# Optimization experiments

Measured on AMD Instinct MI355X. Metric: run time of the kernel, lower is better.

Reference implementation:

```python
import jax, jax.numpy as jnp
import numpy as np

D_MODEL = 2048
N_HEADS = 16
Q_LORA = 1536
KV_LORA = 512
NOPE = 128
ROPE = 64
D_QK = NOPE + ROPE  # 192
D_V = 128
D_FF = 8192
BATCH = 2
SEQ = 2048
THETA = 10000.0
EPS = 1e-5


def rms_norm(x, w=None, eps=EPS):
    y = x * jax.lax.rsqrt(jnp.mean(x * x, axis=-1, keepdims=True) + eps)
    return y * w if w is not None else y


def apply_rope(x, cos, sin):
    # x: [B,S,H,D] with D even; pairs are consecutive (view_as_complex semantics)
    xr, xi = x[..., 0::2], x[..., 1::2]            # [B,S,H,D/2]
    c = cos[None, :, None, :]
    s = sin[None, :, None, :]
    yr = xr * c - xi * s
    yi = xr * s + xi * c
    return jnp.stack([yr, yi], axis=-1).reshape(x.shape)


def setup_inputs() -> dict:
    key = jax.random.key(0)
    ks = jax.random.split(key, 12)
    sd = 0.02
    inv_freq = 1.0 / (THETA ** (np.arange(0, ROPE, 2, dtype=np.float32) / ROPE))
    freqs = np.outer(np.arange(SEQ, dtype=np.float32), inv_freq)  # [S, ROPE/2]
    return {
        "hidden_states": jax.random.normal(ks[0], (BATCH, SEQ, D_MODEL), jnp.float32),
        "sequence_mask": jnp.ones((BATCH, SEQ), jnp.int32),
        "freqs_cos": jnp.asarray(np.cos(freqs)),
        "freqs_sin": jnp.asarray(np.sin(freqs)),
        "ln1_w": jnp.ones((D_MODEL,), jnp.float32),
        "ln2_w": jnp.ones((D_MODEL,), jnp.float32),
        "Wq_down": jax.random.normal(ks[1], (D_MODEL, Q_LORA), jnp.float32) * sd,
        "Wq_up": jax.random.normal(ks[2], (Q_LORA, N_HEADS * D_QK), jnp.float32) * sd,
        "Wkv_down": jax.random.normal(ks[3], (D_MODEL, KV_LORA + ROPE), jnp.float32) * sd,
        "Wkv_up": jax.random.normal(ks[4], (KV_LORA, N_HEADS * (NOPE + D_V)), jnp.float32) * sd,
        "Wo": jax.random.normal(ks[5], (N_HEADS * D_V, D_MODEL), jnp.float32) * sd,
        "Wgate": jax.random.normal(ks[6], (D_MODEL, D_FF), jnp.float32) * sd,
        "Wup": jax.random.normal(ks[7], (D_MODEL, D_FF), jnp.float32) * sd,
        "Wdown": jax.random.normal(ks[8], (D_FF, D_MODEL), jnp.float32) * sd,
    }


def reference(hidden_states, sequence_mask, freqs_cos, freqs_sin, ln1_w, ln2_w,
              Wq_down, Wq_up, Wkv_down, Wkv_up, Wo, Wgate, Wup, Wdown):
    B, S, _ = hidden_states.shape
    residual = hidden_states
    h = rms_norm(hidden_states, ln1_w)

    # --- MLA attention ---
    q_latent = rms_norm(h @ Wq_down)                       # [B,S,q_lora]
    q = (q_latent @ Wq_up).reshape(B, S, N_HEADS, D_QK)
    q_nope, q_rope = q[..., :NOPE], q[..., NOPE:]
    q_rope = apply_rope(q_rope, freqs_cos, freqs_sin)
    q = jnp.concatenate([q_rope, q_nope], axis=-1)         # [B,S,H,192]

    kv_lr = h @ Wkv_down                                   # [B,S,kv_lora+rope]
    kv_latent, k_rope = kv_lr[..., :KV_LORA], kv_lr[..., KV_LORA:]
    k_rope = apply_rope(k_rope[:, :, None, :], freqs_cos, freqs_sin)  # [B,S,1,64]
    k_rope = jnp.broadcast_to(k_rope, (B, S, N_HEADS, ROPE))
    kv = (rms_norm(kv_latent) @ Wkv_up)                    # [B,S,H*(nope+v)]
    k_nope = kv[..., :N_HEADS * NOPE].reshape(B, S, N_HEADS, NOPE)
    v = kv[..., N_HEADS * NOPE:].reshape(B, S, N_HEADS, D_V)
    k = jnp.concatenate([k_rope, k_nope], axis=-1)         # [B,S,H,192]

    scale = 1.0 / jnp.sqrt(jnp.float32(D_QK))
    scores = jnp.einsum('bqhd,bkhd->bhqk', q, k) * scale   # [B,H,S,S]
    seq_ok = (sequence_mask > 0)
    causal = jnp.tril(jnp.ones((S, S), bool))
    mask = causal[None, None] & seq_ok[:, None, None, :]
    scores = jnp.where(mask, scores, jnp.float32(-1e30))
    probs = jax.nn.softmax(scores, axis=-1)
    attn = jnp.einsum('bhqk,bkhd->bqhd', probs, v)         # [B,S,H,128]
    attn_out = attn.reshape(B, S, N_HEADS * D_V) @ Wo

    x = residual + attn_out

    # --- dense GLU MLP ---
    h2 = rms_norm(x, ln2_w)
    mlp_out = (jax.nn.silu(h2 @ Wgate) * (h2 @ Wup)) @ Wdown
    return x + mlp_out
```

## Files before the change

### kernel.cpp

```cpp
#include <hip/hip_runtime.h>
#include <hip/hip_bf16.h>
#include <stdint.h>

#define B_    2
#define S_    2048
#define H_    16
#define DM    2048
#define QL    1536
#define KVL   512
#define NOPE_ 128
#define ROPE_ 64
#define DQK   192
#define DV    128
#define DFF   8192
#define NT    (B_ * S_)
#define EPS_  1e-5f

typedef __bf16 bf16x8 __attribute__((ext_vector_type(8)));
typedef float  f32x4  __attribute__((ext_vector_type(4)));

__device__ __forceinline__ unsigned short f2bf(float f) {
  union { float f; uint32_t u; } v; v.f = f;
  uint32_t r = v.u + 0x7fffu + ((v.u >> 16) & 1u);
  return (unsigned short)(r >> 16);
}
__device__ __forceinline__ float bf2f(unsigned short h) {
  union { uint32_t u; float f; } v; v.u = ((uint32_t)h) << 16;
  return v.f;
}
__device__ __forceinline__ float ldv(float x) { return x; }
__device__ __forceinline__ float ldv(unsigned short x) { return bf2f(x); }

__device__ __forceinline__ void g2l16(const unsigned short* g, unsigned short* l) {
  __builtin_amdgcn_global_load_lds((const __attribute__((address_space(1))) unsigned int*)g,
                                   (__attribute__((address_space(3))) unsigned int*)l,
                                   16, 0, 0);
}

__global__ __launch_bounds__(256) void wt_kernel(const float* __restrict__ W,
                                                 unsigned short* __restrict__ Wt,
                                                 int K, int N) {
  __shared__ unsigned short tile[32][33];
  int kt = blockIdx.y * 32, nt = blockIdx.x * 32;
  int tx = threadIdx.x & 31, ty = threadIdx.x >> 5;
#pragma unroll
  for (int kk = 0; kk < 32; kk += 8)
    tile[kk + ty][tx] = f2bf(W[(size_t)(kt + kk + ty) * N + nt + tx]);
  __syncthreads();
#pragma unroll
  for (int nn = 0; nn < 32; nn += 8)
    Wt[(size_t)(nt + nn + ty) * K + kt + tx] = tile[tx][nn + ty];
}

template <typename TIN>
__global__ __launch_bounds__(256) void rms_kernel(const TIN* __restrict__ in,
                                                  unsigned short* __restrict__ out,
                                                  const float* __restrict__ w,
                                                  int D, int ldin) {
  int row = blockIdx.x, tid = threadIdx.x;
  const TIN* rp = in + (size_t)row * ldin;
  float ss = 0.f;
  for (int i = tid; i < D; i += 256) { float v = ldv(rp[i]); ss += v * v; }
#pragma unroll
  for (int off = 32; off >= 1; off >>= 1) ss += __shfl_xor(ss, off);
  __shared__ float red[4];
  if ((tid & 63) == 0) red[tid >> 6] = ss;
  __syncthreads();
  ss = red[0] + red[1] + red[2] + red[3];
  float rs = rsqrtf(ss / (float)D + EPS_);
  unsigned short* op = out + (size_t)row * D;
  for (int i = tid; i < D; i += 256) {
    float v = ldv(rp[i]) * rs;
    if (w) v *= w[i];
    op[i] = f2bf(v);
  }
}

template <int MODE>
__global__ __launch_bounds__(256) void gemm128(const unsigned short* __restrict__ A,
                                               const unsigned short* __restrict__ Bt,
                                               void* C, const float* __restrict__ addsrc,
                                               int M, int N, int K) {
  __shared__ unsigned short As[128 * 32];
  __shared__ unsigned short Bs[128 * 32];
  int tid = threadIdx.x, lane = tid & 63, wave = tid >> 6;
  int quad = lane >> 4, l16 = lane & 15;
  int wm = wave >> 1, wn = wave & 1;
  int m0 = blockIdx.y * 128, n0 = blockIdx.x * 128;

  int f0 = tid * 8;
  int rs0 = f0 >> 5, cs0 = f0 & 31;
  const unsigned short* Ag0 = A + (size_t)(m0 + rs0) * K + cs0;
  const unsigned short* Ag1 = A + (size_t)(m0 + 64 + rs0) * K + cs0;
  const unsigned short* Bg0 = Bt + (size_t)(n0 + rs0) * K + cs0;
  const unsigned short* Bg1 = Bt + (size_t)(n0 + 64 + rs0) * K + cs0;

  const unsigned short* ArdBase = As + quad * 8 + (wm * 64 + l16) * 32;
  const unsigned short* BrdBase = Bs + quad * 8 + (wn * 64 + l16) * 32;

  f32x4 ac[4][4] = {};
  for (int k = 0; k < K; k += 32) {
    __syncthreads();
    g2l16(Ag0 + k, (unsigned short*)As + f0);
    g2l16(Ag1 + k, (unsigned short*)As + 2048 + f0);
    g2l16(Bg0 + k, (unsigned short*)Bs + f0);
    g2l16(Bg1 + k, (unsigned short*)Bs + 2048 + f0);
    __syncthreads();
    bf16x8 af[4], bfr[4];
#pragma unroll
    for (int mt = 0; mt < 4; ++mt) af[mt]  = *(const bf16x8*)(ArdBase + mt * 16 * 32);
#pragma unroll
    for (int nt = 0; nt < 4; ++nt) bfr[nt] = *(const bf16x8*)(BrdBase + nt * 16 * 32);
#pragma unroll
    for (int mt = 0; mt < 4; ++mt)
#pragma unroll
      for (int nt = 0; nt < 4; ++nt)
        ac[mt][nt] = __builtin_amdgcn_mfma_f32_16x16x32_bf16(af[mt], bfr[nt], ac[mt][nt], 0, 0, 0);
  }

#pragma unroll
  for (int mt = 0; mt < 4; ++mt)
#pragma unroll
    for (int nt = 0; nt < 4; ++nt)
#pragma unroll
      for (int r = 0; r < 4; ++r) {
        int row = m0 + wm * 64 + mt * 16 + quad * 4 + r;
        int col = n0 + wn * 64 + nt * 16 + l16;
        size_t idx = (size_t)row * N + col;
        float v = ac[mt][nt][r];
        if (MODE == 0)      ((unsigned short*)C)[idx] = f2bf(v);
        else if (MODE == 1) ((float*)C)[idx] = v;
        else                ((float*)C)[idx] = addsrc[idx] + v;
      }
}

template <int MODE>
__global__ __launch_bounds__(256) void gemm_kernel(const unsigned short* __restrict__ A,
                                                   const unsigned short* __restrict__ Bt,
                                                   void* C, const float* addsrc,
                                                   int M, int N, int K) {
  int lane = threadIdx.x & 63, wave = threadIdx.x >> 6;
  int quad = lane >> 4, l16 = lane & 15;
  int row0 = blockIdx.y * 64 + wave * 16;
  int col0 = blockIdx.x * 64;
  const unsigned short* Ap = A + (size_t)(row0 + l16) * K + quad * 8;
  const unsigned short* Bp = Bt + (size_t)(col0 + l16) * K + quad * 8;
  size_t bs16 = (size_t)16 * K;
  f32x4 ac[4] = {};
  for (int k = 0; k < K; k += 32) {
    bf16x8 a = *(const bf16x8*)(Ap + k);
#pragma unroll
    for (int t = 0; t < 4; ++t) {
      bf16x8 b = *(const bf16x8*)(Bp + bs16 * t + k);
      ac[t] = __builtin_amdgcn_mfma_f32_16x16x32_bf16(a, b, ac[t], 0, 0, 0);
    }
  }
#pragma unroll
  for (int t = 0; t < 4; ++t)
#pragma unroll
    for (int r = 0; r < 4; ++r) {
      int row = row0 + quad * 4 + r, col = col0 + t * 16 + l16;
      size_t idx = (size_t)row * N + col;
      float v = ac[t][r];
      if (MODE == 0)      ((unsigned short*)C)[idx] = f2bf(v);
      else if (MODE == 1) ((float*)C)[idx] = v;
      else                ((float*)C)[idx] = addsrc[idx] + v;
    }
}

__global__ __launch_bounds__(256) void silumul_kernel(const unsigned short* __restrict__ g,
                                                      const unsigned short* __restrict__ u,
                                                      unsigned short* __restrict__ o, int n8) {
  int i = blockIdx.x * 256 + threadIdx.x;
  if (i >= n8) return;
  uint4 gv = ((const uint4*)g)[i];
  uint4 uv = ((const uint4*)u)[i];
  const unsigned short* gp = (const unsigned short*)&gv;
  const unsigned short* up = (const unsigned short*)&uv;
  uint4 ov;
  unsigned short* op = (unsigned short*)&ov;
#pragma unroll
  for (int j = 0; j < 8; ++j) {
    float gf = bf2f(gp[j]), uf = bf2f(up[j]);
    float s = gf / (1.f + __expf(-gf));
    op[j] = f2bf(s * uf);
  }
  ((uint4*)o)[i] = ov;
}

__global__ __launch_bounds__(256) void build_q_kernel(const unsigned short* __restrict__ qg,
                                                      const float* __restrict__ fcos,
                                                      const float* __restrict__ fsin,
                                                      unsigned short* __restrict__ qo) {
  const float SCALE = 0.07216878364870323f;
  int idx = blockIdx.x * 256 + threadIdx.x;
  if (idx >= NT * H_ * 96) return;
  int i = idx % 96, t = idx / 96;
  int h = t % H_, bs = t / H_, s = bs % S_;
  const unsigned short* src = qg + (size_t)bs * (H_ * DQK) + h * DQK;
  unsigned short* dst = qo + ((size_t)bs * H_ + h) * DQK;
  if (i < 32) {
    float xr = bf2f(src[NOPE_ + 2 * i]), xi = bf2f(src[NOPE_ + 2 * i + 1]);
    float c = fcos[s * 32 + i], sn = fsin[s * 32 + i];
    dst[2 * i]     = f2bf((xr * c - xi * sn) * SCALE);
    dst[2 * i + 1] = f2bf((xr * sn + xi * c) * SCALE);
  } else {
    int j = i - 32;
    dst[ROPE_ + 2 * j]     = f2bf(bf2f(src[2 * j]) * SCALE);
    dst[ROPE_ + 2 * j + 1] = f2bf(bf2f(src[2 * j + 1]) * SCALE);
  }
}

__global__ __launch_bounds__(256) void build_k_kernel(const float* __restrict__ kvlr,
                                                      const unsigned short* __restrict__ kv,
                                                      const float* __restrict__ fcos,
                                                      const float* __restrict__ fsin,
                                                      unsigned short* __restrict__ ko) {
  int idx = blockIdx.x * 256 + threadIdx.x;
  if (idx >= NT * H_ * 96) return;
  int i = idx % 96, t = idx / 96;
  int h = t % H_, bs = t / H_, s = bs % S_;
  unsigned short* dst = ko + ((size_t)bs * H_ + h) * DQK;
  if (i < 32) {
    float xr = kvlr[(size_t)bs * (KVL + ROPE_) + KVL + 2 * i];
    float xi = kvlr[(size_t)bs * (KVL + ROPE_) + KVL + 2 * i + 1];
    float c = fcos[s * 32 + i], sn = fsin[s * 32 + i];
    dst[2 * i]     = f2bf(xr * c - xi * sn);
    dst[2 * i + 1] = f2bf(xr * sn + xi * c);
  } else {
    int j = i - 32;
    dst[ROPE_ + 2 * j]     = kv[(size_t)bs * 4096 + h * DV + 2 * j];
    dst[ROPE_ + 2 * j + 1] = kv[(size_t)bs * 4096 + h * DV + 2 * j + 1];
  }
}

__global__ __launch_bounds__(256) void vt_kernel(const unsigned short* __restrict__ kv,
                                                 unsigned short* __restrict__ vt) {
  __shared__ unsigned short t[32][33];
  int bh = blockIdx.z, b = bh >> 4, h = bh & 15;
  int s0 = blockIdx.x * 32, d0 = blockIdx.y * 32;
  int tx = threadIdx.x & 31, ty = threadIdx.x >> 5;
#pragma unroll
  for (int i = 0; i < 32; i += 8)
    t[i + ty][tx] = kv[(size_t)(b * S_ + s0 + i + ty) * 4096 + 2048 + h * 128 + d0 + tx];
  __syncthreads();
#pragma unroll
  for (int i = 0; i < 32; i += 8)
    vt[((size_t)bh * 128 + d0 + i + ty) * S_ + s0 + tx] = t[tx][i + ty];
}

#define KSTR 200
#define VSTR 40
#define PSTR 40
__global__ __launch_bounds__(256, 2) void attn2_kernel(const unsigned short* __restrict__ Q,
                                                       const unsigned short* __restrict__ Kt,
                                                       const unsigned short* __restrict__ Vt,
                                                       const int* __restrict__ smaskg,
                                                       unsigned short* __restrict__ O) {
  __shared__ unsigned short Ks[32 * KSTR];
  __shared__ unsigned short Vts[128 * VSTR];
  __shared__ unsigned short Ps[4][32 * PSTR];
  __shared__ int smaskl[32];

  int tid = threadIdx.x, wave = tid >> 6, lane = tid & 63;
  int quad = lane >> 4, l16 = lane & 15;
  int bh = blockIdx.y, b = bh >> 4, h = bh & 15;
  int qb = (int)gridDim.x - 1 - (int)blockIdx.x;
  int r0 = qb * 128;

  bf16x8 qf[2][6];
#pragma unroll
  for (int mt = 0; mt < 2; ++mt) {
    int rg = r0 + wave * 32 + mt * 16 + l16;
    const unsigned short* qp = Q + ((size_t)(b * S_ + rg) * H_ + h) * DQK + quad * 8;
#pragma unroll
    for (int kk = 0; kk < 6; ++kk)
      qf[mt][kk] = *(const bf16x8*)(qp + kk * 32);
  }

  float m_[2][4], l_[2][4];
  f32x4 o_[2][8] = {};
#pragma unroll
  for (int mt = 0; mt < 2; ++mt)
#pragma unroll
    for (int r = 0; r < 4; ++r) { m_[mt][r] = -3e38f; l_[mt][r] = 0.f; }

  int ktend = 4 * qb + 4;
  for (int kt = 0; kt < ktend; ++kt) {
    int j0 = kt * 32;
    __syncthreads();
#pragma unroll
    for (int i = 0; i < 3; ++i) {
      int c = tid + i * 256;
      int row = c / 24, cc = (c % 24) * 8;
      *(uint4*)(Ks + row * KSTR + cc) =
          *(const uint4*)(Kt + ((size_t)(b * S_ + j0 + row) * H_ + h) * DQK + cc);
    }
#pragma unroll
    for (int i = 0; i < 2; ++i) {
      int c = tid + i * 256;
      int d = c >> 2, cc = (c & 3) * 8;
      *(uint4*)(Vts + d * VSTR + cc) =
          *(const uint4*)(Vt + ((size_t)bh * 128 + d) * S_ + j0 + cc);
    }
    if (tid < 32) smaskl[tid] = smaskg[b * S_ + j0 + tid];
    __syncthreads();

    f32x4 sc[2][2] = {};
#pragma unroll
    for (int kk = 0; kk < 6; ++kk) {
      bf16x8 b0 = *(const bf16x8*)(Ks + l16 * KSTR + kk * 32 + quad * 8);
      bf16x8 b1 = *(const bf16x8*)(Ks + (16 + l16) * KSTR + kk * 32 + quad * 8);
#pragma unroll
      for (int mt = 0; mt < 2; ++mt) {
        sc[mt][0] = __builtin_amdgcn_mfma_f32_16x16x32_bf16(qf[mt][kk], b0, sc[mt][0], 0, 0, 0);
        sc[mt][1] = __builtin_amdgcn_mfma_f32_16x16x32_bf16(qf[mt][kk], b1, sc[mt][1], 0, 0, 0);
      }
    }

    bool ok0 = smaskl[l16] != 0, ok1 = smaskl[16 + l16] != 0;
    int c0 = j0 + l16, c1 = j0 + 16 + l16;
#pragma unroll
    for (int mt = 0; mt < 2; ++mt) {
      int rbase = r0 + wave * 32 + mt * 16 + quad * 4;
#pragma unroll
      for (int r = 0; r < 4; ++r) {
        int rg = rbase + r;
        float s0 = (ok0 && c0 <= rg) ? sc[mt][0][r] : -1e30f;
        float s1 = (ok1 && c1 <= rg) ? sc[mt][1][r] : -1e30f;
        float tm = fmaxf(s0, s1);
        tm = fmaxf(tm, __shfl_xor(tm, 1));
        tm = fmaxf(tm, __shfl_xor(tm, 2));
        tm = fmaxf(tm, __shfl_xor(tm, 4));
        tm = fmaxf(tm, __shfl_xor(tm, 8));
        float mn = fmaxf(m_[mt][r], tm);
        float al = __expf(m_[mt][r] - mn);
        m_[mt][r] = mn;
        float p0 = __expf(s0 - mn);
        float p1 = __expf(s1 - mn);
        float ps = p0 + p1;
        ps += __shfl_xor(ps, 1);
        ps += __shfl_xor(ps, 2);
        ps += __shfl_xor(ps, 4);
        ps += __shfl_xor(ps, 8);
        l_[mt][r] = l_[mt][r] * al + ps;
#pragma unroll
        for (int nt = 0; nt < 8; ++nt) o_[mt][nt][r] *= al;
        int prow = mt * 16 + quad * 4 + r;
        Ps[wave][prow * PSTR + l16]      = f2bf(p0);
        Ps[wave][prow * PSTR + 16 + l16] = f2bf(p1);
      }
    }

    bf16x8 pa[2];
#pragma unroll
    for (int mt = 0; mt < 2; ++mt)
      pa[mt] = *(const bf16x8*)(&Ps[wave][(mt * 16 + l16) * PSTR + quad * 8]);
#pragma unroll
    for (int nt = 0; nt < 8; ++nt) {
      bf16x8 vb = *(const bf16x8*)(Vts + (nt * 16 + l16) * VSTR + quad * 8);
#pragma unroll
      for (int mt = 0; mt < 2; ++mt)
        o_[mt][nt] = __builtin_amdgcn_mfma_f32_16x16x32_bf16(pa[mt], vb, o_[mt][nt], 0, 0, 0);
    }
  }

#pragma unroll
  for (int mt = 0; mt < 2; ++mt)
#pragma unroll
    for (int nt = 0; nt < 8; ++nt)
#pragma unroll
      for (int r = 0; r < 4; ++r) {
        int rg = r0 + wave * 32 + mt * 16 + quad * 4 + r;
        float v = o_[mt][nt][r] / l_[mt][r];
        O[((size_t)(b * S_ + rg) * H_ + h) * DV + nt * 16 + l16] = f2bf(v);
      }
}

extern "C" void kernel_launch(void* const* d_in, const int* in_sizes, int n_in,
                              void* d_out, int out_size, void* d_ws, size_t ws_size,
                              hipStream_t stream) {
  const float* hidden  = (const float*)d_in[0];
  const int*   seqmask = (const int*)d_in[1];
  const float* fcos    = (const float*)d_in[2];
  const float* fsin    = (const float*)d_in[3];
  const float* ln1     = (const float*)d_in[4];
  const float* ln2     = (const float*)d_in[5];
  const float* Wqd     = (const float*)d_in[6];
  const float* Wqu     = (const float*)d_in[7];
  const float* Wkvd    = (const float*)d_in[8];
  const float* Wkvu    = (const float*)d_in[9];
  const float* Wo      = (const float*)d_in[10];
  const float* Wg      = (const float*)d_in[11];
  const float* Wu      = (const float*)d_in[12];
  const float* Wd      = (const float*)d_in[13];
  float* out = (float*)d_out;
  char* ws = (char*)d_ws;

  size_t off = 0;
  unsigned short* Wqd_t  = (unsigned short*)(ws + off); off += (size_t)QL * DM * 2;
  unsigned short* Wqu_t  = (unsigned short*)(ws + off); off += (size_t)(H_ * DQK) * QL * 2;
  unsigned short* Wkvd_t = (unsigned short*)(ws + off); off += (size_t)(KVL + ROPE_) * DM * 2;
  unsigned short* Wkvu_t = (unsigned short*)(ws + off); off += (size_t)4096 * KVL * 2;
  unsigned short* Wo_t   = (unsigned short*)(ws + off); off += (size_t)DM * DM * 2;
  unsigned short* Wg_t   = (unsigned short*)(ws + off); off += (size_t)DFF * DM * 2;
  unsigned short* Wu_t   = (unsigned short*)(ws + off); off += (size_t)DFF * DM * 2;
  unsigned short* Wd_t   = (unsigned short*)(ws + off); off += (size_t)DM * DFF * 2;
  char* scr = ws + off;

  unsigned short* h_bf   = (unsigned short*)(scr + 0);
  unsigned short* qdown  = (unsigned short*)(scr + 16777216);
  float*          kvlr   = (float*)(scr + 29360128);
  unsigned short* qlat   = (unsigned short*)(scr + 0);
  unsigned short* qgemm  = (unsigned short*)(scr + 38797312);
  unsigned short* kvnorm = (unsigned short*)(scr + 63963136);
  unsigned short* kv     = (unsigned short*)(scr + 68157440);
  unsigned short* qattn  = (unsigned short*)(scr + 0);
  unsigned short* kattn  = (unsigned short*)(scr + 38797312);
  unsigned short* attn   = (unsigned short*)(scr + 101711872);
  unsigned short* vt     = (unsigned short*)(scr + 118489088);
  unsigned short* h2     = (unsigned short*)(scr + 0);
  unsigned short* gbuf   = (unsigned short*)(scr + 16777216);
  unsigned short* ubuf   = (unsigned short*)(scr + 83886080);

  auto T = [&](const float* W, unsigned short* Wt, int K, int N) {
    wt_kernel<<<dim3(N / 32, K / 32), 256, 0, stream>>>(W, Wt, K, N);
  };
  T(Wqd, Wqd_t, DM, QL);
  T(Wqu, Wqu_t, QL, H_ * DQK);
  T(Wkvd, Wkvd_t, DM, KVL + ROPE_);
  T(Wkvu, Wkvu_t, KVL, 4096);
  T(Wo, Wo_t, DM, DM);
  T(Wg, Wg_t, DM, DFF);
  T(Wu, Wu_t, DM, DFF);
  T(Wd, Wd_t, DFF, DM);

  rms_kernel<float><<<NT, 256, 0, stream>>>(hidden, h_bf, ln1, DM, DM);
  gemm128<0><<<dim3(QL / 128, NT / 128), 256, 0, stream>>>(h_bf, Wqd_t, qdown, nullptr, NT, QL, DM);
  gemm_kernel<1><<<dim3((KVL + ROPE_) / 64, NT / 64), 256, 0, stream>>>(h_bf, Wkvd_t, kvlr, nullptr, NT, KVL + ROPE_, DM);
  rms_kernel<unsigned short><<<NT, 256, 0, stream>>>(qdown, qlat, nullptr, QL, QL);
  gemm128<0><<<dim3(H_ * DQK / 128, NT / 128), 256, 0, stream>>>(qlat, Wqu_t, qgemm, nullptr, NT, H_ * DQK, QL);
  rms_kernel<float><<<NT, 256, 0, stream>>>(kvlr, kvnorm, nullptr, KVL, KVL + ROPE_);
  gemm128<0><<<dim3(4096 / 128, NT / 128), 256, 0, stream>>>(kvnorm, Wkvu_t, kv, nullptr, NT, 4096, KVL);
  int nbq = (NT * H_ * 96 + 255) / 256;
  build_q_kernel<<<nbq, 256, 0, stream>>>(qgemm, fcos, fsin, qattn);
  build_k_kernel<<<nbq, 256, 0, stream>>>(kvlr, kv, fcos, fsin, kattn);
  vt_kernel<<<dim3(S_ / 32, DV / 32, B_ * H_), 256, 0, stream>>>(kv, vt);
  attn2_kernel<<<dim3(S_ / 128, B_ * H_), 256, 0, stream>>>(qattn, kattn, vt, seqmask, attn);
  gemm128<2><<<dim3(DM / 128, NT / 128), 256, 0, stream>>>(attn, Wo_t, out, hidden, NT, DM, DM);
  rms_kernel<float><<<NT, 256, 0, stream>>>(out, h2, ln2, DM, DM);
  gemm128<0><<<dim3(DFF / 128, NT / 128), 256, 0, stream>>>(h2, Wg_t, gbuf, nullptr, NT, DFF, DM);
  gemm128<0><<<dim3(DFF / 128, NT / 128), 256, 0, stream>>>(h2, Wu_t, ubuf, nullptr, NT, DFF, DM);
  silumul_kernel<<<(NT * DFF / 8 + 255) / 256, 256, 0, stream>>>(gbuf, ubuf, gbuf, NT * DFF / 8);
  gemm128<2><<<dim3(DM / 128, NT / 128), 256, 0, stream>>>(gbuf, Wd_t, out, out, NT, DM, DFF);

  (void)in_sizes; (void)n_in; (void)out_size; (void)ws_size;
}
```

Baseline: 1.566 ms.

## Double-buffer GEMM LDS tiles, fuse SiLU-mul into up GEMM, pad KV-down GEMM

The 128x128 GEMM now uses two LDS buffers: the next K-slice is prefetched asynchronously while MFMAs run on the current one, which removes one barrier per iteration and overlaps loads with compute. A new epilogue mode applies SiLU to the gate buffer and multiplies it by the up-projection result in place. This drops the separate up buffer and the elementwise kernel. The KV-down projection is padded to 640 columns so it can use the tiled GEMM instead of the naive one. The padded weight rows are never written, so the extra output columns hold garbage but are ignored. Doubling LDS use may lower occupancy.

```diff
diff --git a/kernel.cpp b/kernel.cpp
--- a/kernel.cpp
+++ b/kernel.cpp
@@ -15,6 +15,7 @@
 #define DFF   8192
 #define NT    (B_ * S_)
 #define EPS_  1e-5f
+#define KVLP  640
 
 typedef __bf16 bf16x8 __attribute__((ext_vector_type(8)));
 typedef float  f32x4  __attribute__((ext_vector_type(4)));
@@ -79,10 +80,10 @@
 template <int MODE>
 __global__ __launch_bounds__(256) void gemm128(const unsigned short* __restrict__ A,
                                                const unsigned short* __restrict__ Bt,
-                                               void* C, const float* __restrict__ addsrc,
+                                               void* C, const void* __restrict__ aux,
                                                int M, int N, int K) {
-  __shared__ unsigned short As[128 * 32];
-  __shared__ unsigned short Bs[128 * 32];
+  __shared__ unsigned short As[2][128 * 32];
+  __shared__ unsigned short Bs[2][128 * 32];
   int tid = threadIdx.x, lane = tid & 63, wave = tid >> 6;
   int quad = lane >> 4, l16 = lane & 15;
   int wm = wave >> 1, wn = wave & 1;
@@ -95,17 +96,24 @@
   const unsigned short* Bg0 = Bt + (size_t)(n0 + rs0) * K + cs0;
   const unsigned short* Bg1 = Bt + (size_t)(n0 + 64 + rs0) * K + cs0;
 
-  const unsigned short* ArdBase = As + quad * 8 + (wm * 64 + l16) * 32;
-  const unsigned short* BrdBase = Bs + quad * 8 + (wn * 64 + l16) * 32;
+  g2l16(Ag0, As[0] + f0);
+  g2l16(Ag1, As[0] + 2048 + f0);
+  g2l16(Bg0, Bs[0] + f0);
+  g2l16(Bg1, Bs[0] + 2048 + f0);
 
   f32x4 ac[4][4] = {};
+  int p = 0;
   for (int k = 0; k < K; k += 32) {
     __syncthreads();
-    g2l16(Ag0 + k, (unsigned short*)As + f0);
-    g2l16(Ag1 + k, (unsigned short*)As + 2048 + f0);
-    g2l16(Bg0 + k, (unsigned short*)Bs + f0);
-    g2l16(Bg1 + k, (unsigned short*)Bs + 2048 + f0);
-    __syncthreads();
+    int k2 = k + 32;
+    if (k2 < K) {
+      g2l16(Ag0 + k2, As[p ^ 1] + f0);
+      g2l16(Ag1 + k2, As[p ^ 1] + 2048 + f0);
+      g2l16(Bg0 + k2, Bs[p ^ 1] + f0);
+      g2l16(Bg1 + k2, Bs[p ^ 1] + 2048 + f0);
+    }
+    const unsigned short* ArdBase = As[p] + quad * 8 + (wm * 64 + l16) * 32;
+    const unsigned short* BrdBase = Bs[p] + quad * 8 + (wn * 64 + l16) * 32;
     bf16x8 af[4], bfr[4];
 #pragma unroll
     for (int mt = 0; mt < 4; ++mt) af[mt]  = *(const bf16x8*)(ArdBase + mt * 16 * 32);
@@ -116,6 +124,7 @@
 #pragma unroll
       for (int nt = 0; nt < 4; ++nt)
         ac[mt][nt] = __builtin_amdgcn_mfma_f32_16x16x32_bf16(af[mt], bfr[nt], ac[mt][nt], 0, 0, 0);
+    p ^= 1;
   }
 
 #pragma unroll
@@ -130,62 +139,13 @@
         float v = ac[mt][nt][r];
         if (MODE == 0)      ((unsigned short*)C)[idx] = f2bf(v);
         else if (MODE == 1) ((float*)C)[idx] = v;
-        else                ((float*)C)[idx] = addsrc[idx] + v;
+        else if (MODE == 2) ((float*)C)[idx] = ((const float*)aux)[idx] + v;
+        else {
+          float g = bf2f(((const unsigned short*)aux)[idx]);
+          float s = g / (1.f + __expf(-g));
+          ((unsigned short*)C)[idx] = f2bf(s * v);
+        }
       }
-}
-
-template <int MODE>
-__global__ __launch_bounds__(256) void gemm_kernel(const unsigned short* __restrict__ A,
-                                                   const unsigned short* __restrict__ Bt,
-                                                   void* C, const float* addsrc,
-                                                   int M, int N, int K) {
-  int lane = threadIdx.x & 63, wave = threadIdx.x >> 6;
-  int quad = lane >> 4, l16 = lane & 15;
-  int row0 = blockIdx.y * 64 + wave * 16;
-  int col0 = blockIdx.x * 64;
-  const unsigned short* Ap = A + (size_t)(row0 + l16) * K + quad * 8;
-  const unsigned short* Bp = Bt + (size_t)(col0 + l16) * K + quad * 8;
-  size_t bs16 = (size_t)16 * K;
-  f32x4 ac[4] = {};
-  for (int k = 0; k < K; k += 32) {
-    bf16x8 a = *(const bf16x8*)(Ap + k);
-#pragma unroll
-    for (int t = 0; t < 4; ++t) {
-      bf16x8 b = *(const bf16x8*)(Bp + bs16 * t + k);
-      ac[t] = __builtin_amdgcn_mfma_f32_16x16x32_bf16(a, b, ac[t], 0, 0, 0);
-    }
-  }
-#pragma unroll
-  for (int t = 0; t < 4; ++t)
-#pragma unroll
-    for (int r = 0; r < 4; ++r) {
-      int row = row0 + quad * 4 + r, col = col0 + t * 16 + l16;
-      size_t idx = (size_t)row * N + col;
-      float v = ac[t][r];
-      if (MODE == 0)      ((unsigned short*)C)[idx] = f2bf(v);
-      else if (MODE == 1) ((float*)C)[idx] = v;
-      else                ((float*)C)[idx] = addsrc[idx] + v;
-    }
-}
-
-__global__ __launch_bounds__(256) void silumul_kernel(const unsigned short* __restrict__ g,
-                                                      const unsigned short* __restrict__ u,
-                                                      unsigned short* __restrict__ o, int n8) {
-  int i = blockIdx.x * 256 + threadIdx.x;
-  if (i >= n8) return;
-  uint4 gv = ((const uint4*)g)[i];
-  uint4 uv = ((const uint4*)u)[i];
-  const unsigned short* gp = (const unsigned short*)&gv;
-  const unsigned short* up = (const unsigned short*)&uv;
-  uint4 ov;
-  unsigned short* op = (unsigned short*)&ov;
-#pragma unroll
-  for (int j = 0; j < 8; ++j) {
-    float gf = bf2f(gp[j]), uf = bf2f(up[j]);
-    float s = gf / (1.f + __expf(-gf));
-    op[j] = f2bf(s * uf);
-  }
-  ((uint4*)o)[i] = ov;
 }
 
 __global__ __launch_bounds__(256) void build_q_kernel(const unsigned short* __restrict__ qg,
@@ -222,8 +182,8 @@
   int h = t % H_, bs = t / H_, s = bs % S_;
   unsigned short* dst = ko + ((size_t)bs * H_ + h) * DQK;
   if (i < 32) {
-    float xr = kvlr[(size_t)bs * (KVL + ROPE_) + KVL + 2 * i];
-    float xi = kvlr[(size_t)bs * (KVL + ROPE_) + KVL + 2 * i + 1];
+    float xr = kvlr[(size_t)bs * KVLP + KVL + 2 * i];
+    float xi = kvlr[(size_t)bs * KVLP + KVL + 2 * i + 1];
     float c = fcos[s * 32 + i], sn = fsin[s * 32 + i];
     dst[2 * i]     = f2bf(xr * c - xi * sn);
     dst[2 * i + 1] = f2bf(xr * sn + xi * c);
@@ -400,7 +360,7 @@
   size_t off = 0;
   unsigned short* Wqd_t  = (unsigned short*)(ws + off); off += (size_t)QL * DM * 2;
   unsigned short* Wqu_t  = (unsigned short*)(ws + off); off += (size_t)(H_ * DQK) * QL * 2;
-  unsigned short* Wkvd_t = (unsigned short*)(ws + off); off += (size_t)(KVL + ROPE_) * DM * 2;
+  unsigned short* Wkvd_t = (unsigned short*)(ws + off); off += (size_t)KVLP * DM * 2;
   unsigned short* Wkvu_t = (unsigned short*)(ws + off); off += (size_t)4096 * KVL * 2;
   unsigned short* Wo_t   = (unsigned short*)(ws + off); off += (size_t)DM * DM * 2;
   unsigned short* Wg_t   = (unsigned short*)(ws + off); off += (size_t)DFF * DM * 2;
@@ -412,16 +372,15 @@
   unsigned short* qdown  = (unsigned short*)(scr + 16777216);
   float*          kvlr   = (float*)(scr + 29360128);
   unsigned short* qlat   = (unsigned short*)(scr + 0);
-  unsigned short* qgemm  = (unsigned short*)(scr + 38797312);
-  unsigned short* kvnorm = (unsigned short*)(scr + 63963136);
-  unsigned short* kv     = (unsigned short*)(scr + 68157440);
+  unsigned short* qgemm  = (unsigned short*)(scr + 39845888);
+  unsigned short* kvnorm = (unsigned short*)(scr + 65011712);
+  unsigned short* kv     = (unsigned short*)(scr + 69206016);
   unsigned short* qattn  = (unsigned short*)(scr + 0);
-  unsigned short* kattn  = (unsigned short*)(scr + 38797312);
-  unsigned short* attn   = (unsigned short*)(scr + 101711872);
-  unsigned short* vt     = (unsigned short*)(scr + 118489088);
+  unsigned short* kattn  = (unsigned short*)(scr + 39845888);
+  unsigned short* attn   = (unsigned short*)(scr + 102760448);
+  unsigned short* vt     = (unsigned short*)(scr + 119537664);
   unsigned short* h2     = (unsigned short*)(scr + 0);
   unsigned short* gbuf   = (unsigned short*)(scr + 16777216);
-  unsigned short* ubuf   = (unsigned short*)(scr + 83886080);
 
   auto T = [&](const float* W, unsigned short* Wt, int K, int N) {
     wt_kernel<<<dim3(N / 32, K / 32), 256, 0, stream>>>(W, Wt, K, N);
@@ -437,10 +396,10 @@
 
   rms_kernel<float><<<NT, 256, 0, stream>>>(hidden, h_bf, ln1, DM, DM);
   gemm128<0><<<dim3(QL / 128, NT / 128), 256, 0, stream>>>(h_bf, Wqd_t, qdown, nullptr, NT, QL, DM);
-  gemm_kernel<1><<<dim3((KVL + ROPE_) / 64, NT / 64), 256, 0, stream>>>(h_bf, Wkvd_t, kvlr, nullptr, NT, KVL + ROPE_, DM);
+  gemm128<1><<<dim3(KVLP / 128, NT / 128), 256, 0, stream>>>(h_bf, Wkvd_t, kvlr, nullptr, NT, KVLP, DM);
   rms_kernel<unsigned short><<<NT, 256, 0, stream>>>(qdown, qlat, nullptr, QL, QL);
   gemm128<0><<<dim3(H_ * DQK / 128, NT / 128), 256, 0, stream>>>(qlat, Wqu_t, qgemm, nullptr, NT, H_ * DQK, QL);
-  rms_kernel<float><<<NT, 256, 0, stream>>>(kvlr, kvnorm, nullptr, KVL, KVL + ROPE_);
+  rms_kernel<float><<<NT, 256, 0, stream>>>(kvlr, kvnorm, nullptr, KVL, KVLP);
   gemm128<0><<<dim3(4096 / 128, NT / 128), 256, 0, stream>>>(kvnorm, Wkvu_t, kv, nullptr, NT, 4096, KVL);
   int nbq = (NT * H_ * 96 + 255) / 256;
   build_q_kernel<<<nbq, 256, 0, stream>>>(qgemm, fcos, fsin, qattn);
@@ -450,8 +409,7 @@
   gemm128<2><<<dim3(DM / 128, NT / 128), 256, 0, stream>>>(attn, Wo_t, out, hidden, NT, DM, DM);
   rms_kernel<float><<<NT, 256, 0, stream>>>(out, h2, ln2, DM, DM);
   gemm128<0><<<dim3(DFF / 128, NT / 128), 256, 0, stream>>>(h2, Wg_t, gbuf, nullptr, NT, DFF, DM);
-  gemm128<0><<<dim3(DFF / 128, NT / 128), 256, 0, stream>>>(h2, Wu_t, ubuf, nullptr, NT, DFF, DM);
-  silumul_kernel<<<(NT * DFF / 8 + 255) / 256, 256, 0, stream>>>(gbuf, ubuf, gbuf, NT * DFF / 8);
+  gemm128<3><<<dim3(DFF / 128, NT / 128), 256, 0, stream>>>(h2, Wu_t, gbuf, gbuf, NT, DFF, DM);
   gemm128<2><<<dim3(DM / 128, NT / 128), 256, 0, stream>>>(gbuf, Wd_t, out, out, NT, DM, DFF);
 
   (void)in_sizes; (void)n_in; (void)out_size; (void)ws_size;
```

New measurement: 1.471 ms. 1.06x faster.
